# Performance work log

Hardware: AMD Instinct MI355X
Metric: run time of the kernel (lower is better)

Reference implementation:

```python
import jax, jax.numpy as jnp
import numpy as np

E, H, F, LE, LD, K, CD, DIN = 256, 8, 1024, 4, 3, 8, 4, 4
B, S = 16, 512
SIG2 = 1.0 ** 2 + 1e-8   # dr_sigma**2 + 1e-8
EPS = 1e-5               # LayerNorm / BatchNorm eps


def _ln(x, w, b):
    m = x.mean(-1, keepdims=True)
    v = ((x - m) ** 2).mean(-1, keepdims=True)
    return (x - m) / jnp.sqrt(v + EPS) * w + b


def _gelu(x):
    return jax.nn.gelu(x, approximate=False)  # torch nn.GELU default = exact erf


def _mha(xq, xkv, qkv_w, qkv_b, out_w, out_b, bias=None):
    # torch nn.MultiheadAttention (batch_first), additive float attn bias broadcast over heads
    wq, wk, wv = jnp.split(qkv_w, 3, axis=0)
    bq, bk, bv = jnp.split(qkv_b, 3)
    q = xq @ wq.T + bq
    k = xkv @ wk.T + bk
    v = xkv @ wv.T + bv
    Bn, Tq, Tk = q.shape[0], q.shape[1], k.shape[1]
    hd = E // H
    qh = q.reshape(Bn, Tq, H, hd)
    kh = k.reshape(Bn, Tk, H, hd)
    vh = v.reshape(Bn, Tk, H, hd)
    s = jnp.einsum('bqhd,bkhd->bhqk', qh, kh) / jnp.sqrt(jnp.asarray(hd, q.dtype))
    if bias is not None:
        s = s + bias[:, None]  # same bias for every head
    p = jax.nn.softmax(s, axis=-1)
    o = jnp.einsum('bhqk,bkhd->bqhd', p, vh).reshape(Bn, Tq, E)
    return o @ out_w.T + out_b


def _forward(x, mask, parent_idx, in_w, in_b, bn_w, bn_b, dr_gamma,
             e_qkv_w, e_qkv_b, e_out_w, e_out_b, e_l1_w, e_l1_b, e_l2_w, e_l2_b,
             e_n1_w, e_n1_b, e_n2_w, e_n2_b,
             parent_w, parent_b, query_embed, c1_w, c1_b, c2_w, c2_b,
             d_sqkv_w, d_sqkv_b, d_sout_w, d_sout_b,
             d_cqkv_w, d_cqkv_b, d_cout_w, d_cout_b,
             d_l1_w, d_l1_b, d_l2_w, d_l2_b,
             d_n1_w, d_n1_b, d_n2_w, d_n2_b, d_n3_w, d_n3_b,
             child_w, child_b, o1_w, o1_b, o2_w, o2_b):
    x = jnp.nan_to_num(x)
    # input_dim==4 convention: (log_pt, dEta, dPhi, log_E)
    coords = jnp.stack([x[..., 1], x[..., 2]], axis=-1)          # [B,S,2]
    # input_proj: Linear -> BatchNorm1d (eval: mean 0, var 1) -> GELU (dropout=identity in eval)
    h = x @ in_w.T + in_b
    h = (h / jnp.sqrt(1.0 + EPS)) * bn_w + bn_b
    h = _gelu(h)
    # dR Gaussian attention bias: [B,S,S]; mask is all-valid so no -inf fill
    d = coords[:, :, None, :] - coords[:, None, :, :]
    dr2 = d[..., 0] ** 2 + d[..., 1] ** 2
    bias = -(dr_gamma[0] * dr2) / (2.0 * SIG2)
    # dR-biased pre-norm encoder
    for i in range(LE):
        hn = _ln(h, e_n1_w[i], e_n1_b[i])
        h = h + _mha(hn, hn, e_qkv_w[i], e_qkv_b[i], e_out_w[i], e_out_b[i], bias)
        hn = _ln(h, e_n2_w[i], e_n2_b[i])
        h = h + _gelu(hn @ e_l1_w[i].T + e_l1_b[i]) @ e_l2_w[i].T + e_l2_b[i]
    memory = jnp.nan_to_num(h)
    parent_logit = (memory @ parent_w.T + parent_b)[..., 0]       # [B,S]
    # conditional decoder queries
    p = memory[jnp.arange(memory.shape[0]), parent_idx]           # [B,E]
    m = mask.astype(memory.dtype)
    g = (memory * m[..., None]).sum(1) / jnp.maximum(m.sum(1, keepdims=True), 1.0)
    cond = _gelu(jnp.concatenate([p, g], -1) @ c1_w.T + c1_b) @ c2_w.T + c2_b
    t = query_embed[None] + cond[:, None]                         # [B,K,E]
    # pre-norm transformer decoder (self-attn, cross-attn, ff)
    for i in range(LD):
        tn = _ln(t, d_n1_w[i], d_n1_b[i])
        t = t + _mha(tn, tn, d_sqkv_w[i], d_sqkv_b[i], d_sout_w[i], d_sout_b[i])
        tn = _ln(t, d_n2_w[i], d_n2_b[i])
        t = t + _mha(tn, memory, d_cqkv_w[i], d_cqkv_b[i], d_cout_w[i], d_cout_b[i])
        tn = _ln(t, d_n3_w[i], d_n3_b[i])
        t = t + _gelu(tn @ d_l1_w[i].T + d_l1_b[i]) @ d_l2_w[i].T + d_l2_b[i]
    child_feat = t @ child_w.T + child_b                          # [B,K,CD]
    obj_logit = (_gelu(t @ o1_w.T + o1_b) @ o2_w.T + o2_b)[..., 0]  # [B,K]
    return parent_logit, child_feat, obj_logit


def setup_inputs() -> dict:
    key = jax.random.key(0)
    ks = iter(jax.random.split(key, 64))
    def w(shape, scale=0.05):
        return jax.random.normal(next(ks), shape, jnp.float32) * scale
    return {
        'x': jax.random.normal(next(ks), (B, S, DIN), jnp.float32),
        'mask': jnp.ones((B, S), dtype=bool),
        'parent_idx': jax.random.randint(next(ks), (B,), 0, S),
        'in_w': w((E, DIN)), 'in_b': jnp.zeros((E,)),
        'bn_w': jnp.ones((E,)), 'bn_b': jnp.zeros((E,)),
        'dr_gamma': jnp.ones((1,)),
        'e_qkv_w': w((LE, 3 * E, E)), 'e_qkv_b': jnp.zeros((LE, 3 * E)),
        'e_out_w': w((LE, E, E)), 'e_out_b': jnp.zeros((LE, E)),
        'e_l1_w': w((LE, F, E)), 'e_l1_b': jnp.zeros((LE, F)),
        'e_l2_w': w((LE, E, F)), 'e_l2_b': jnp.zeros((LE, E)),
        'e_n1_w': jnp.ones((LE, E)), 'e_n1_b': jnp.zeros((LE, E)),
        'e_n2_w': jnp.ones((LE, E)), 'e_n2_b': jnp.zeros((LE, E)),
        'parent_w': w((1, E)), 'parent_b': jnp.zeros((1,)),
        'query_embed': w((K, E), 0.02),
        'c1_w': w((E, 2 * E)), 'c1_b': jnp.zeros((E,)),
        'c2_w': w((E, E)), 'c2_b': jnp.zeros((E,)),
        'd_sqkv_w': w((LD, 3 * E, E)), 'd_sqkv_b': jnp.zeros((LD, 3 * E)),
        'd_sout_w': w((LD, E, E)), 'd_sout_b': jnp.zeros((LD, E)),
        'd_cqkv_w': w((LD, 3 * E, E)), 'd_cqkv_b': jnp.zeros((LD, 3 * E)),
        'd_cout_w': w((LD, E, E)), 'd_cout_b': jnp.zeros((LD, E)),
        'd_l1_w': w((LD, F, E)), 'd_l1_b': jnp.zeros((LD, F)),
        'd_l2_w': w((LD, E, F)), 'd_l2_b': jnp.zeros((LD, E)),
        'd_n1_w': jnp.ones((LD, E)), 'd_n1_b': jnp.zeros((LD, E)),
        'd_n2_w': jnp.ones((LD, E)), 'd_n2_b': jnp.zeros((LD, E)),
        'd_n3_w': jnp.ones((LD, E)), 'd_n3_b': jnp.zeros((LD, E)),
        'child_w': w((CD, E)), 'child_b': jnp.zeros((CD,)),
        'o1_w': w((E, E)), 'o1_b': jnp.zeros((E,)),
        'o2_w': w((1, E)), 'o2_b': jnp.zeros((1,)),
    }


def reference(x, mask, parent_idx, in_w, in_b, bn_w, bn_b, dr_gamma,
              e_qkv_w, e_qkv_b, e_out_w, e_out_b, e_l1_w, e_l1_b, e_l2_w, e_l2_b,
              e_n1_w, e_n1_b, e_n2_w, e_n2_b,
              parent_w, parent_b, query_embed, c1_w, c1_b, c2_w, c2_b,
              d_sqkv_w, d_sqkv_b, d_sout_w, d_sout_b,
              d_cqkv_w, d_cqkv_b, d_cout_w, d_cout_b,
              d_l1_w, d_l1_b, d_l2_w, d_l2_b,
              d_n1_w, d_n1_b, d_n2_w, d_n2_b, d_n3_w, d_n3_b,
              child_w, child_b, o1_w, o1_b, o2_w, o2_b):
    return _forward(x, mask, parent_idx, in_w, in_b, bn_w, bn_b, dr_gamma,
                    e_qkv_w, e_qkv_b, e_out_w, e_out_b, e_l1_w, e_l1_b, e_l2_w, e_l2_b,
                    e_n1_w, e_n1_b, e_n2_w, e_n2_b,
                    parent_w, parent_b, query_embed, c1_w, c1_b, c2_w, c2_b,
                    d_sqkv_w, d_sqkv_b, d_sout_w, d_sout_b,
                    d_cqkv_w, d_cqkv_b, d_cout_w, d_cout_b,
                    d_l1_w, d_l1_b, d_l2_w, d_l2_b,
                    d_n1_w, d_n1_b, d_n2_w, d_n2_b, d_n3_w, d_n3_b,
                    child_w, child_b, o1_w, o1_b, o2_w, o2_b)
```

## Files before the change

### kernel.cpp

```cpp
#include <hip/hip_runtime.h>
#include <math.h>

#define E 256
#define H 8
#define HD 32
#define FF 1024
#define LE 4
#define LDN 3
#define KQ 8
#define CDIM 4
#define DIN 4
#define BATCH 16
#define SEQ 512

typedef __attribute__((ext_vector_type(8))) short s8b;
typedef __attribute__((ext_vector_type(4))) float f32x4;

__device__ __forceinline__ float gelu_f(float x) {
  return 0.5f * x * (1.f + erff(x * 0.70710678118654752f));
}

__device__ __forceinline__ unsigned short f2b(float f) {
  union { float f; unsigned u; } a;
  a.f = f;
  unsigned r = (a.u + 0x7fffu + ((a.u >> 16) & 1u)) >> 16;
  return (unsigned short)r;
}

template <int GELU, int RESID, int OMODE>
__global__ __launch_bounds__(256) void mfma_gemm_kernel(
    const unsigned short* __restrict__ A, const unsigned short* __restrict__ Wt,
    const float* __restrict__ bias, const float* __restrict__ resid,
    float* __restrict__ outf, unsigned short* __restrict__ outb,
    unsigned short* __restrict__ vtb,
    int M, int N, int K) {
  __shared__ unsigned short As[128 * 32];
  __shared__ unsigned short Bs[128 * 32];
  int tid = threadIdx.x;
  int lane = tid & 63, w = tid >> 6;
  int row0 = blockIdx.y * 128, col0 = blockIdx.x * 128;
  int wr = (w >> 1) * 64, wc = (w & 1) * 64;
  f32x4 acc[4][4] = {};
  int sr = tid >> 2;
  int sc = tid & 3;
  const unsigned short* Ap = A + (size_t)(row0 + sr) * K + sc * 8;
  const unsigned short* Bp = Wt + (size_t)(col0 + sr) * K + sc * 8;
  int xw = (sc ^ ((sr >> 1) & 3)) * 8;
  int w0 = sr * 32 + xw;
  int w1 = (sr + 64) * 32 + xw;

  for (int k0 = 0; k0 < K; k0 += 32) {
    s8b a0 = *(const s8b*)(Ap + k0);
    s8b a1 = *(const s8b*)(Ap + (size_t)64 * K + k0);
    s8b b0 = *(const s8b*)(Bp + k0);
    s8b b1 = *(const s8b*)(Bp + (size_t)64 * K + k0);
    __syncthreads();
    *(s8b*)(As + w0) = a0;
    *(s8b*)(As + w1) = a1;
    *(s8b*)(Bs + w0) = b0;
    *(s8b*)(Bs + w1) = b1;
    __syncthreads();
    int krow = lane & 15, kq = lane >> 4;
    s8b afr[4], bfr[4];
    #pragma unroll
    for (int mi = 0; mi < 4; ++mi) {
      int r = wr + mi * 16 + krow;
      afr[mi] = *(const s8b*)(As + r * 32 + ((kq ^ ((r >> 1) & 3)) * 8));
    }
    #pragma unroll
    for (int ni = 0; ni < 4; ++ni) {
      int r = wc + ni * 16 + krow;
      bfr[ni] = *(const s8b*)(Bs + r * 32 + ((kq ^ ((r >> 1) & 3)) * 8));
    }
    #pragma unroll
    for (int mi = 0; mi < 4; ++mi)
      #pragma unroll
      for (int ni = 0; ni < 4; ++ni)
        acc[mi][ni] = __builtin_amdgcn_mfma_f32_16x16x32_bf16(afr[mi], bfr[ni], acc[mi][ni], 0, 0, 0);
  }

  int cl = lane & 15, rb = (lane >> 4) * 4;
  #pragma unroll
  for (int ni = 0; ni < 4; ++ni) {
    int col = col0 + wc + ni * 16 + cl;
    float bv = bias[col];
    #pragma unroll
    for (int mi = 0; mi < 4; ++mi) {
      #pragma unroll
      for (int j = 0; j < 4; ++j) {
        int row = row0 + wr + mi * 16 + rb + j;
        float v = acc[mi][ni][j] + bv;
        if (RESID) v += resid[(size_t)row * N + col];
        if (GELU) v = gelu_f(v);
        if (OMODE == 0) {
          outf[(size_t)row * N + col] = v;
        } else if (OMODE == 1) {
          outb[(size_t)row * N + col] = f2b(v);
        } else {
          int b = row >> 9, s = row & 511;
          int sect = col >> 8, hh = (col >> 5) & 7, d = col & 31;
          if (sect < 2)
            outb[((((size_t)sect * BATCH + b) * H + hh) * SEQ + s) * HD + d] = f2b(v);
          else
            vtb[(((size_t)b * H + hh) * HD + d) * SEQ + s] = f2b(v);
        }
      }
    }
  }
}

__global__ __launch_bounds__(256) void mfma_attn_kernel(
    const unsigned short* __restrict__ qkb, const unsigned short* __restrict__ vt,
    const float2* __restrict__ carr, const float* __restrict__ gamma_p,
    unsigned short* __restrict__ out) {
  __shared__ __align__(16) unsigned short P[4][16 * 64];
  int tid = threadIdx.x, lane = tid & 63, w = tid >> 6;
  int qt = blockIdx.x, h = blockIdx.y, b = blockIdx.z;
  int q0 = qt * 64 + w * 16;
  const unsigned short* qh = qkb + (((size_t)b * H + h) * SEQ) * HD;
  const unsigned short* kh = qkb + ((((size_t)BATCH + b) * H + h) * SEQ) * HD;
  const unsigned short* vh = vt + (((size_t)b * H + h) * HD) * SEQ;
  int r16 = lane & 15, q4 = lane >> 4;
  s8b qa = *(const s8b*)(qh + (size_t)(q0 + r16) * HD + q4 * 8);
  float eq[4], pq[4];
  #pragma unroll
  for (int j = 0; j < 4; ++j) {
    float2 c = carr[b * SEQ + q0 + q4 * 4 + j];
    eq[j] = c.x; pq[j] = c.y;
  }
  float gam = gamma_p[0] * 0.49999999500000004f;
  const float scale = 0.17677669529663687f;
  float m[4], lsum[4];
  #pragma unroll
  for (int j = 0; j < 4; ++j) { m[j] = -1e30f; lsum[j] = 0.f; }
  f32x4 o0 = {}, o1 = {};
  const f32x4 zf = {0.f, 0.f, 0.f, 0.f};
  unsigned short* pw = &P[w][0];

  for (int t = 0; t < SEQ / 64; ++t) {
    int k0 = t * 64;
    f32x4 sf[4];
    #pragma unroll
    for (int f = 0; f < 4; ++f) {
      s8b bk = *(const s8b*)(kh + (size_t)(k0 + f * 16 + r16) * HD + q4 * 8);
      sf[f] = __builtin_amdgcn_mfma_f32_16x16x32_bf16(qa, bk, zf, 0, 0, 0);
    }
    float ek[4], pk[4];
    #pragma unroll
    for (int f = 0; f < 4; ++f) {
      float2 c = carr[b * SEQ + k0 + f * 16 + r16];
      ek[f] = c.x; pk[f] = c.y;
    }
    float sc_[4][4];
    float tmax[4] = {-1e30f, -1e30f, -1e30f, -1e30f};
    #pragma unroll
    for (int f = 0; f < 4; ++f)
      #pragma unroll
      for (int j = 0; j < 4; ++j) {
        float de = eq[j] - ek[f], dp = pq[j] - pk[f];
        float v = sf[f][j] * scale - gam * (de * de + dp * dp);
        sc_[f][j] = v;
        tmax[j] = fmaxf(tmax[j], v);
      }
    #pragma unroll
    for (int j = 0; j < 4; ++j) {
      #pragma unroll
      for (int off = 1; off < 16; off <<= 1)
        tmax[j] = fmaxf(tmax[j], __shfl_xor(tmax[j], off));
      float mn = fmaxf(m[j], tmax[j]);
      float al = __expf(m[j] - mn);
      m[j] = mn;
      lsum[j] *= al;
      o0[j] *= al;
      o1[j] *= al;
    }
    __syncthreads();
    #pragma unroll
    for (int f = 0; f < 4; ++f)
      #pragma unroll
      for (int j = 0; j < 4; ++j) {
        float p = __expf(sc_[f][j] - m[j]);
        lsum[j] += p;
        int prow = q4 * 4 + j;
        int c = f * 16 + r16;
        int chunk = (c >> 3) ^ (prow & 7);
        pw[prow * 64 + chunk * 8 + (c & 7)] = f2b(p);
      }
    __syncthreads();
    #pragma unroll
    for (int ks = 0; ks < 2; ++ks) {
      int chunk = (ks * 4 + q4) ^ (r16 & 7);
      s8b pa = *(const s8b*)(pw + r16 * 64 + chunk * 8);
      s8b v0 = *(const s8b*)(vh + (size_t)r16 * SEQ + k0 + ks * 32 + q4 * 8);
      s8b v1 = *(const s8b*)(vh + (size_t)(16 + r16) * SEQ + k0 + ks * 32 + q4 * 8);
      o0 = __builtin_amdgcn_mfma_f32_16x16x32_bf16(pa, v0, o0, 0, 0, 0);
      o1 = __builtin_amdgcn_mfma_f32_16x16x32_bf16(pa, v1, o1, 0, 0, 0);
    }
  }
  #pragma unroll
  for (int j = 0; j < 4; ++j) {
    #pragma unroll
    for (int off = 1; off < 16; off <<= 1)
      lsum[j] += __shfl_xor(lsum[j], off);
    float inv = 1.f / lsum[j];
    size_t rbase = ((size_t)(b * SEQ + q0 + q4 * 4 + j)) * E + h * HD;
    out[rbase + r16] = f2b(o0[j] * inv);
    out[rbase + 16 + r16] = f2b(o1[j] * inv);
  }
}

__global__ void coords_kernel(const float* __restrict__ x, float2* __restrict__ carr) {
  int i = blockIdx.x * 256 + threadIdx.x;
  if (i >= BATCH * SEQ) return;
  carr[i] = make_float2(x[(size_t)i * DIN + 1], x[(size_t)i * DIN + 2]);
}

__global__ void f2b_kernel(const float* __restrict__ in, unsigned short* __restrict__ out, int n4) {
  int i = blockIdx.x * 256 + threadIdx.x;
  if (i >= n4) return;
  float4 v = ((const float4*)in)[i];
  ushort4 o;
  o.x = f2b(v.x); o.y = f2b(v.y); o.z = f2b(v.z); o.w = f2b(v.w);
  ((ushort4*)out)[i] = o;
}


template <int N, int GELU>
__global__ __launch_bounds__(256) void dec_ln_gemv_kernel(
    const float* __restrict__ t, const float* __restrict__ nw, const float* __restrict__ nb,
    const float* __restrict__ W, const float* __restrict__ bias, float* __restrict__ outg) {
  __shared__ float X[8][256];
  __shared__ float Pp[4][64][9];
  int b = blockIdx.x, by = blockIdx.y, tid = threadIdx.x;
  const float* tg = t + (size_t)b * 2048;
  int w = tid >> 6, l = tid & 63;
  #pragma unroll
  for (int rr = 0; rr < 2; ++rr) {
    int r = w * 2 + rr;
    float v0 = tg[r * 256 + l], v1 = tg[r * 256 + 64 + l];
    float v2 = tg[r * 256 + 128 + l], v3 = tg[r * 256 + 192 + l];
    float s = v0 + v1 + v2 + v3;
    for (int o = 32; o > 0; o >>= 1) s += __shfl_xor(s, o);
    float mean = s * (1.f / 256);
    float d0 = v0 - mean, d1 = v1 - mean, d2 = v2 - mean, d3 = v3 - mean;
    float var = d0 * d0 + d1 * d1 + d2 * d2 + d3 * d3;
    for (int o = 32; o > 0; o >>= 1) var += __shfl_xor(var, o);
    float inv = rsqrtf(var * (1.f / 256) + 1e-5f);
    X[r][l] = d0 * inv * nw[l] + nb[l];
    X[r][l + 64] = d1 * inv * nw[l + 64] + nb[l + 64];
    X[r][l + 128] = d2 * inv * nw[l + 128] + nb[l + 128];
    X[r][l + 192] = d3 * inv * nw[l + 192] + nb[l + 192];
  }
  __syncthreads();
  int j = tid & 63, kq = tid >> 6;
  int col = by * 64 + j;
  const float4* wp = (const float4*)(W + (size_t)col * 256 + kq * 64);
  float acc[8] = {};
  #pragma unroll
  for (int kk = 0; kk < 16; ++kk) {
    float4 wv = wp[kk];
    int base = kq * 64 + kk * 4;
    #pragma unroll
    for (int r = 0; r < 8; ++r) {
      float4 xv = *(const float4*)&X[r][base];
      acc[r] += xv.x * wv.x + xv.y * wv.y + xv.z * wv.z + xv.w * wv.w;
    }
  }
  #pragma unroll
  for (int r = 0; r < 8; ++r) Pp[kq][j][r] = acc[r];
  __syncthreads();
  for (int i = tid; i < 512; i += 256) {
    int r = i & 7, j2 = i >> 3;
    float v = Pp[0][j2][r] + Pp[1][j2][r] + Pp[2][j2][r] + Pp[3][j2][r] + bias[by * 64 + j2];
    if (GELU) v = gelu_f(v);
    outg[((size_t)b * 8 + r) * N + by * 64 + j2] = v;
  }
}

__global__ __launch_bounds__(256) void dec_gemv_resid_kernel(
    const float* __restrict__ Xg, const float* __restrict__ W, const float* __restrict__ bias,
    float* __restrict__ t) {
  __shared__ float X[8][256];
  __shared__ float Pp[4][64][9];
  int b = blockIdx.x, by = blockIdx.y, tid = threadIdx.x;
  const float* xg = Xg + (size_t)b * 2048;
  for (int i = tid; i < 2048; i += 256) ((float*)X)[i] = xg[i];
  __syncthreads();
  int j = tid & 63, kq = tid >> 6;
  int col = by * 64 + j;
  const float4* wp = (const float4*)(W + (size_t)col * 256 + kq * 64);
  float acc[8] = {};
  #pragma unroll
  for (int kk = 0; kk < 16; ++kk) {
    float4 wv = wp[kk];
    int base = kq * 64 + kk * 4;
    #pragma unroll
    for (int r = 0; r < 8; ++r) {
      float4 xv = *(const float4*)&X[r][base];
      acc[r] += xv.x * wv.x + xv.y * wv.y + xv.z * wv.z + xv.w * wv.w;
    }
  }
  #pragma unroll
  for (int r = 0; r < 8; ++r) Pp[kq][j][r] = acc[r];
  __syncthreads();
  for (int i = tid; i < 512; i += 256) {
    int r = i & 7, j2 = i >> 3;
    float v = Pp[0][j2][r] + Pp[1][j2][r] + Pp[2][j2][r] + Pp[3][j2][r] + bias[by * 64 + j2];
    t[((size_t)b * 8 + r) * 256 + by * 64 + j2] += v;
  }
}

__global__ __launch_bounds__(256) void dec_ffn2_kernel(
    const float* __restrict__ MIDg, const float* __restrict__ W, const float* __restrict__ bias,
    float* __restrict__ t) {
  __shared__ float X[8][1024];
  __shared__ float Pp[4][64][9];
  int b = blockIdx.x, by = blockIdx.y, tid = threadIdx.x;
  const float* xg = MIDg + (size_t)b * 8192;
  for (int i = tid; i < 8192; i += 256) ((float*)X)[i] = xg[i];
  __syncthreads();
  int j = tid & 63, kq = tid >> 6;
  int col = by * 64 + j;
  const float4* wp = (const float4*)(W + (size_t)col * 1024 + kq * 256);
  float acc[8] = {};
  #pragma unroll 8
  for (int kk = 0; kk < 64; ++kk) {
    float4 wv = wp[kk];
    int base = kq * 256 + kk * 4;
    #pragma unroll
    for (int r = 0; r < 8; ++r) {
      float4 xv = *(const float4*)&X[r][base];
      acc[r] += xv.x * wv.x + xv.y * wv.y + xv.z * wv.z + xv.w * wv.w;
    }
  }
  #pragma unroll
  for (int r = 0; r < 8; ++r) Pp[kq][j][r] = acc[r];
  __syncthreads();
  for (int i = tid; i < 512; i += 256) {
    int r = i & 7, j2 = i >> 3;
    float v = Pp[0][j2][r] + Pp[1][j2][r] + Pp[2][j2][r] + Pp[3][j2][r] + bias[by * 64 + j2];
    t[((size_t)b * 8 + r) * 256 + by * 64 + j2] += v;
  }
}

__global__ __launch_bounds__(256) void dec_selfattn_kernel(
    const float* __restrict__ qkvg, float* __restrict__ ao) {
  __shared__ float QK[8][768];
  __shared__ float S[512];
  int b = blockIdx.x, tid = threadIdx.x;
  const float* qg = qkvg + (size_t)b * 8 * 768;
  for (int i = tid; i < 6144; i += 256) ((float*)QK)[i] = qg[i];
  __syncthreads();
  for (int t2 = tid; t2 < 512; t2 += 256) {
    int h = t2 >> 6, q = (t2 >> 3) & 7, k = t2 & 7;
    const float* qp = &QK[q][h * 32];
    const float* kp = &QK[k][256 + h * 32];
    float d = 0.f;
    #pragma unroll
    for (int jj = 0; jj < 32; ++jj) d += qp[jj] * kp[jj];
    S[t2] = d * 0.17677669529663687f;
  }
  __syncthreads();
  if (tid < 64) {
    float* row = &S[tid * 8];
    float m = row[0];
    #pragma unroll
    for (int k = 1; k < 8; ++k) m = fmaxf(m, row[k]);
    float sum = 0.f;
    #pragma unroll
    for (int k = 0; k < 8; ++k) { float e = __expf(row[k] - m); row[k] = e; sum += e; }
    float inv = 1.f / sum;
    #pragma unroll
    for (int k = 0; k < 8; ++k) row[k] *= inv;
  }
  __syncthreads();
  for (int i = tid; i < 2048; i += 256) {
    int q = i >> 8, c = i & 255, h = c >> 5;
    const float* pr = &S[h * 64 + q * 8];
    float acc = 0.f;
    #pragma unroll
    for (int k = 0; k < 8; ++k) acc += pr[k] * QK[k][512 + c];
    ao[(size_t)b * 2048 + i] = acc;
  }
}

__global__ void cross_attn_kernel(const float* __restrict__ Q,
                                  const float* __restrict__ KV,
                                  float* __restrict__ out) {
  __shared__ float sv[512];
  __shared__ float red[256];
  __shared__ float qv[32];
  __shared__ float pvred[8][32];
  int tid = threadIdx.x;
  int bid = blockIdx.x;
  int q = bid % KQ;
  int h = (bid / KQ) % H;
  int b = bid / (KQ * H);
  if (tid < 32) qv[tid] = Q[((size_t)(b * KQ + q)) * E + h * HD + tid];
  __syncthreads();
  const float scale = 0.17677669529663687f;
  for (int k = tid; k < SEQ; k += 256) {
    const float* kp = KV + ((size_t)(b * SEQ + k)) * 512 + h * HD;
    float d = 0.f;
    #pragma unroll
    for (int j = 0; j < HD; ++j) d += qv[j] * kp[j];
    sv[k] = d * scale;
  }
  __syncthreads();
  float m = -1e30f;
  for (int k = tid; k < SEQ; k += 256) m = fmaxf(m, sv[k]);
  red[tid] = m; __syncthreads();
  for (int s = 128; s > 0; s >>= 1) {
    if (tid < s) red[tid] = fmaxf(red[tid], red[tid + s]);
    __syncthreads();
  }
  m = red[0]; __syncthreads();
  float lsum = 0.f;
  for (int k = tid; k < SEQ; k += 256) { float e = __expf(sv[k] - m); sv[k] = e; lsum += e; }
  red[tid] = lsum; __syncthreads();
  for (int s = 128; s > 0; s >>= 1) {
    if (tid < s) red[tid] += red[tid + s];
    __syncthreads();
  }
  float denom = red[0];
  int d = tid & 31, g = tid >> 5;
  float acc = 0.f;
  for (int k = g; k < SEQ; k += 8)
    acc += sv[k] * KV[((size_t)(b * SEQ + k)) * 512 + 256 + h * HD + d];
  pvred[g][d] = acc;
  __syncthreads();
  if (tid < 32) {
    float r = 0.f;
    #pragma unroll
    for (int gg = 0; gg < 8; ++gg) r += pvred[gg][tid];
    out[((size_t)(b * KQ + q)) * E + h * HD + tid] = r / denom;
  }
}

__global__ void ln_bf16_kernel(const float* __restrict__ in, const float* __restrict__ w,
                               const float* __restrict__ b, unsigned short* __restrict__ out) {
  int r = blockIdx.x;
  int l = threadIdx.x;
  const float* p = in + (size_t)r * E;
  float v0 = p[l], v1 = p[l + 64], v2 = p[l + 128], v3 = p[l + 192];
  float s = v0 + v1 + v2 + v3;
  for (int off = 32; off > 0; off >>= 1) s += __shfl_xor(s, off);
  float mean = s * (1.f / E);
  float d0 = v0 - mean, d1 = v1 - mean, d2 = v2 - mean, d3 = v3 - mean;
  float var = d0 * d0 + d1 * d1 + d2 * d2 + d3 * d3;
  for (int off = 32; off > 0; off >>= 1) var += __shfl_xor(var, off);
  float inv = rsqrtf(var * (1.f / E) + 1e-5f);
  unsigned short* o = out + (size_t)r * E;
  o[l]       = f2b(d0 * inv * w[l]       + b[l]);
  o[l + 64]  = f2b(d1 * inv * w[l + 64]  + b[l + 64]);
  o[l + 128] = f2b(d2 * inv * w[l + 128] + b[l + 128]);
  o[l + 192] = f2b(d3 * inv * w[l + 192] + b[l + 192]);
}

__global__ void input_proj_kernel(const float* __restrict__ x, const float* __restrict__ in_w,
                                  const float* __restrict__ in_b, const float* __restrict__ bn_w,
                                  const float* __restrict__ bn_b, float* __restrict__ h) {
  int idx = blockIdx.x * 256 + threadIdx.x;
  int row = idx >> 8, e = idx & 255;
  const float* xr = x + (size_t)row * DIN;
  float v = in_b[e];
  #pragma unroll
  for (int i = 0; i < DIN; ++i) v += xr[i] * in_w[e * DIN + i];
  v = v * (1.0f / sqrtf(1.0f + 1e-5f)) * bn_w[e] + bn_b[e];
  h[idx] = gelu_f(v);
}

__global__ void pool_gather_kernel(const float* __restrict__ mem, const int* __restrict__ pidx,
                                   float* __restrict__ pg) {
  int b = blockIdx.x, e = threadIdx.x;
  int pi = pidx[b];
  pg[(size_t)b * 512 + e] = mem[((size_t)b * SEQ + pi) * E + e];
  float s = 0.f;
  #pragma unroll 8
  for (int ss = 0; ss < SEQ; ++ss) s += mem[((size_t)b * SEQ + ss) * E + e];
  pg[(size_t)b * 512 + 256 + e] = s * (1.f / SEQ);
}

__global__ void cond_kernel(const float* __restrict__ pg, const float* __restrict__ c1w,
                            const float* __restrict__ c1b, const float* __restrict__ c2w,
                            const float* __restrict__ c2b, const float* __restrict__ qe,
                            float* __restrict__ t) {
  __shared__ float PG[512];
  __shared__ float C1[256];
  int b = blockIdx.x, c = threadIdx.x;
  PG[c] = pg[(size_t)b * 512 + c];
  PG[c + 256] = pg[(size_t)b * 512 + 256 + c];
  __syncthreads();
  const float4* wp = (const float4*)(c1w + (size_t)c * 512);
  float acc = c1b[c];
  #pragma unroll 8
  for (int kk = 0; kk < 128; ++kk) {
    float4 wv = wp[kk];
    int base = kk * 4;
    acc += PG[base] * wv.x + PG[base + 1] * wv.y + PG[base + 2] * wv.z + PG[base + 3] * wv.w;
  }
  C1[c] = gelu_f(acc);
  __syncthreads();
  const float4* wp2 = (const float4*)(c2w + (size_t)c * 256);
  float acc2 = c2b[c];
  #pragma unroll 8
  for (int kk = 0; kk < 64; ++kk) {
    float4 wv = wp2[kk];
    int base = kk * 4;
    acc2 += C1[base] * wv.x + C1[base + 1] * wv.y + C1[base + 2] * wv.z + C1[base + 3] * wv.w;
  }
  #pragma unroll
  for (int k = 0; k < KQ; ++k)
    t[((size_t)b * KQ + k) * E + c] = qe[k * E + c] + acc2;
}

__global__ void head_kernel(const float* __restrict__ t,
                            const float* __restrict__ childw, const float* __restrict__ childb,
                            const float* __restrict__ o1w, const float* __restrict__ o1b,
                            const float* __restrict__ o2w, const float* __restrict__ o2b,
                            float* __restrict__ out_child, float* __restrict__ out_obj) {
  __shared__ float tr[256];
  __shared__ float red[256];
  int r = blockIdx.x, c = threadIdx.x;
  tr[c] = t[(size_t)r * E + c];
  __syncthreads();
  const float4* wp = (const float4*)(o1w + (size_t)c * 256);
  float acc = o1b[c];
  #pragma unroll 8
  for (int kk = 0; kk < 64; ++kk) {
    float4 wv = wp[kk];
    int base = kk * 4;
    acc += tr[base] * wv.x + tr[base + 1] * wv.y + tr[base + 2] * wv.z + tr[base + 3] * wv.w;
  }
  red[c] = gelu_f(acc) * o2w[c];
  __syncthreads();
  for (int s = 128; s > 0; s >>= 1) {
    if (c < s) red[c] += red[c + s];
    __syncthreads();
  }
  if (c == 0) out_obj[r] = red[0] + o2b[0];
  __syncthreads();
  #pragma unroll
  for (int j = 0; j < CDIM; ++j) {
    red[c] = tr[c] * childw[j * E + c];
    __syncthreads();
    for (int s = 128; s > 0; s >>= 1) {
      if (c < s) red[c] += red[c + s];
      __syncthreads();
    }
    if (c == 0) out_child[r * CDIM + j] = red[0] + childb[j];
    __syncthreads();
  }
}

__global__ void rowdot_kernel(const float* __restrict__ A, const float* __restrict__ w,
                              const float* __restrict__ bias, float* __restrict__ out) {
  int r = blockIdx.x, l = threadIdx.x;
  const float* p = A + (size_t)r * E;
  float s = p[l] * w[l] + p[l + 64] * w[l + 64] + p[l + 128] * w[l + 128] + p[l + 192] * w[l + 192];
  for (int off = 32; off > 0; off >>= 1) s += __shfl_xor(s, off);
  if (l == 0) out[r] = s + bias[0];
}

extern "C" void kernel_launch(void* const* d_in, const int* in_sizes, int n_in,
                              void* d_out, int out_size, void* d_ws, size_t ws_size,
                              hipStream_t stream) {
  const float* x          = (const float*)d_in[0];
  const int*   parent_idx = (const int*)d_in[2];
  const float* in_w  = (const float*)d_in[3];
  const float* in_b  = (const float*)d_in[4];
  const float* bn_w  = (const float*)d_in[5];
  const float* bn_b  = (const float*)d_in[6];
  const float* dr_gamma = (const float*)d_in[7];
  const float* e_qkv_w = (const float*)d_in[8];
  const float* e_qkv_b = (const float*)d_in[9];
  const float* e_out_w = (const float*)d_in[10];
  const float* e_out_b = (const float*)d_in[11];
  const float* e_l1_w = (const float*)d_in[12];
  const float* e_l1_b = (const float*)d_in[13];
  const float* e_l2_w = (const float*)d_in[14];
  const float* e_l2_b = (const float*)d_in[15];
  const float* e_n1_w = (const float*)d_in[16];
  const float* e_n1_b = (const float*)d_in[17];
  const float* e_n2_w = (const float*)d_in[18];
  const float* e_n2_b = (const float*)d_in[19];
  const float* parent_w = (const float*)d_in[20];
  const float* parent_b = (const float*)d_in[21];
  const float* query_embed = (const float*)d_in[22];
  const float* c1_w = (const float*)d_in[23];
  const float* c1_b = (const float*)d_in[24];
  const float* c2_w = (const float*)d_in[25];
  const float* c2_b = (const float*)d_in[26];
  const float* d_sqkv_w = (const float*)d_in[27];
  const float* d_sqkv_b = (const float*)d_in[28];
  const float* d_sout_w = (const float*)d_in[29];
  const float* d_sout_b = (const float*)d_in[30];
  const float* d_cqkv_w = (const float*)d_in[31];
  const float* d_cqkv_b = (const float*)d_in[32];
  const float* d_cout_w = (const float*)d_in[33];
  const float* d_cout_b = (const float*)d_in[34];
  const float* d_l1_w = (const float*)d_in[35];
  const float* d_l1_b = (const float*)d_in[36];
  const float* d_l2_w = (const float*)d_in[37];
  const float* d_l2_b = (const float*)d_in[38];
  const float* d_n1_w = (const float*)d_in[39];
  const float* d_n1_b = (const float*)d_in[40];
  const float* d_n2_w = (const float*)d_in[41];
  const float* d_n2_b = (const float*)d_in[42];
  const float* d_n3_w = (const float*)d_in[43];
  const float* d_n3_b = (const float*)d_in[44];
  const float* child_w = (const float*)d_in[45];
  const float* child_b = (const float*)d_in[46];
  const float* o1_w = (const float*)d_in[47];
  const float* o1_b = (const float*)d_in[48];
  const float* o2_w = (const float*)d_in[49];
  const float* o2_b = (const float*)d_in[50];

  float* out = (float*)d_out;
  const int ROWS = BATCH * SEQ;
  const int TROWS = BATCH * KQ;

  float* ws = (float*)d_ws;
  float* h         = ws;
  float* kvbuf     = h + (size_t)ROWS * E;
  float* attnout_d = kvbuf + (size_t)ROWS * 2 * E;
  float* pg        = attnout_d + (size_t)TROWS * E;
  float* tbuf      = pg + BATCH * 2 * E;
  float* q_t       = tbuf + (size_t)TROWS * E;
  float* qkv_t     = q_t + (size_t)TROWS * E;
  float* dmid      = qkv_t + (size_t)TROWS * 3 * E;
  unsigned short* hn_bf   = (unsigned short*)(dmid + (size_t)TROWS * FF);
  unsigned short* attn_bf = hn_bf + (size_t)ROWS * E;
  unsigned short* mid_bf  = attn_bf + (size_t)ROWS * E;
  unsigned short* eqkv_bf = mid_bf + (size_t)ROWS * FF;
  unsigned short* eout_bf = eqkv_bf + (size_t)LE * 3 * E * E;
  unsigned short* el1_bf  = eout_bf + (size_t)LE * E * E;
  unsigned short* el2_bf  = el1_bf + (size_t)LE * FF * E;
  unsigned short* dckv_bf = el2_bf + (size_t)LE * E * FF;
  float2* carr = (float2*)(dckv_bf + (size_t)LDN * 3 * E * E);
  unsigned short* qkb = mid_bf;
  unsigned short* vtb = mid_bf + (size_t)2 * ROWS * E;

  auto cvt = [&](const float* src, unsigned short* dst, size_t n) {
    int n4 = (int)(n / 4);
    f2b_kernel<<<(n4 + 255) / 256, 256, 0, stream>>>(src, dst, n4);
  };

  cvt(e_qkv_w, eqkv_bf, (size_t)LE * 3 * E * E);
  cvt(e_out_w, eout_bf, (size_t)LE * E * E);
  cvt(e_l1_w, el1_bf, (size_t)LE * FF * E);
  cvt(e_l2_w, el2_bf, (size_t)LE * E * FF);
  cvt(d_cqkv_w, dckv_bf, (size_t)LDN * 3 * E * E);
  coords_kernel<<<(BATCH * SEQ + 255) / 256, 256, 0, stream>>>(x, carr);

  input_proj_kernel<<<ROWS, 256, 0, stream>>>(x, in_w, in_b, bn_w, bn_b, h);

  for (int i = 0; i < LE; ++i) {
    const float* qb = e_qkv_b + (size_t)i * 3 * E;
    const float* ob = e_out_b + (size_t)i * E;
    const float* l1b = e_l1_b + (size_t)i * FF;
    const float* l2b = e_l2_b + (size_t)i * E;
    ln_bf16_kernel<<<ROWS, 64, 0, stream>>>(h, e_n1_w + i * E, e_n1_b + i * E, hn_bf);
    mfma_gemm_kernel<0, 0, 2><<<dim3(6, 64), 256, 0, stream>>>(
        hn_bf, eqkv_bf + (size_t)i * 3 * E * E, qb, nullptr, nullptr, qkb, vtb, ROWS, 3 * E, E);
    mfma_attn_kernel<<<dim3(SEQ / 64, H, BATCH), 256, 0, stream>>>(qkb, vtb, carr, dr_gamma, attn_bf);
    mfma_gemm_kernel<0, 1, 0><<<dim3(2, 64), 256, 0, stream>>>(
        attn_bf, eout_bf + (size_t)i * E * E, ob, h, h, nullptr, nullptr, ROWS, E, E);
    ln_bf16_kernel<<<ROWS, 64, 0, stream>>>(h, e_n2_w + i * E, e_n2_b + i * E, hn_bf);
    mfma_gemm_kernel<1, 0, 1><<<dim3(8, 64), 256, 0, stream>>>(
        hn_bf, el1_bf + (size_t)i * FF * E, l1b, nullptr, nullptr, mid_bf, nullptr, ROWS, FF, E);
    mfma_gemm_kernel<0, 1, 0><<<dim3(2, 64), 256, 0, stream>>>(
        mid_bf, el2_bf + (size_t)i * E * FF, l2b, h, h, nullptr, nullptr, ROWS, E, FF);
  }

  rowdot_kernel<<<ROWS, 64, 0, stream>>>(h, parent_w, parent_b, out);

  pool_gather_kernel<<<BATCH, 256, 0, stream>>>(h, parent_idx, pg);
  cond_kernel<<<BATCH, 256, 0, stream>>>(pg, c1_w, c1_b, c2_w, c2_b, query_embed, tbuf);

  cvt(h, hn_bf, (size_t)ROWS * E);

  for (int i = 0; i < LDN; ++i) {
    const float* cqb = d_cqkv_b + (size_t)i * 3 * E;
    mfma_gemm_kernel<0, 0, 0><<<dim3(4, 64), 256, 0, stream>>>(
        hn_bf, dckv_bf + (size_t)i * 3 * E * E + (size_t)E * E, cqb + E, nullptr,
        kvbuf, nullptr, nullptr, ROWS, 2 * E, E);
    dec_ln_gemv_kernel<768, 0><<<dim3(BATCH, 12), 256, 0, stream>>>(
        tbuf, d_n1_w + i * E, d_n1_b + i * E,
        d_sqkv_w + (size_t)i * 3 * E * E, d_sqkv_b + (size_t)i * 3 * E, qkv_t);
    dec_selfattn_kernel<<<BATCH, 256, 0, stream>>>(qkv_t, attnout_d);
    dec_gemv_resid_kernel<<<dim3(BATCH, 4), 256, 0, stream>>>(
        attnout_d, d_sout_w + (size_t)i * E * E, d_sout_b + (size_t)i * E, tbuf);
    dec_ln_gemv_kernel<256, 0><<<dim3(BATCH, 4), 256, 0, stream>>>(
        tbuf, d_n2_w + i * E, d_n2_b + i * E,
        d_cqkv_w + (size_t)i * 3 * E * E, cqb, q_t);
    cross_attn_kernel<<<BATCH * H * KQ, 256, 0, stream>>>(q_t, kvbuf, attnout_d);
    dec_gemv_resid_kernel<<<dim3(BATCH, 4), 256, 0, stream>>>(
        attnout_d, d_cout_w + (size_t)i * E * E, d_cout_b + (size_t)i * E, tbuf);
    dec_ln_gemv_kernel<1024, 1><<<dim3(BATCH, 16), 256, 0, stream>>>(
        tbuf, d_n3_w + i * E, d_n3_b + i * E,
        d_l1_w + (size_t)i * FF * E, d_l1_b + (size_t)i * FF, dmid);
    dec_ffn2_kernel<<<dim3(BATCH, 4), 256, 0, stream>>>(
        dmid, d_l2_w + (size_t)i * E * FF, d_l2_b + (size_t)i * E, tbuf);
  }

  head_kernel<<<TROWS, 256, 0, stream>>>(tbuf, child_w, child_b, o1_w, o1_b, o2_w, o2_b,
                                         out + ROWS, out + ROWS + TROWS * CDIM);
}
```

Before: 866.1 us.

## Use direct global-to-LDS loads, batch decoder KV GEMMs, parallelize pooling

The GEMM tile loads now use global_load_lds to write straight into shared memory, with the swizzle moved to the global address side, so staging no longer passes through registers. The three decoder cross-attention K/V projections are merged into one wide GEMM over remapped bf16 weights, and cross-attention indexes them by stride and offset. The mean-pool/gather kernel is split across feature chunks to use more blocks. The direct LDS loads depend on correct lane-to-address mapping, and the merged GEMM adds a larger fp32 buffer.

```diff
diff --git a/kernel.cpp b/kernel.cpp
--- a/kernel.cpp
+++ b/kernel.cpp
@@ -27,6 +27,11 @@
   return (unsigned short)r;
 }
 
+__device__ __forceinline__ void gload16(const unsigned short* g, unsigned short* l) {
+  __builtin_amdgcn_global_load_lds((const __attribute__((address_space(1))) void*)g,
+                                   (__attribute__((address_space(3))) void*)l, 16, 0, 0);
+}
+
 template <int GELU, int RESID, int OMODE>
 __global__ __launch_bounds__(256) void mfma_gemm_kernel(
     const unsigned short* __restrict__ A, const unsigned short* __restrict__ Wt,
@@ -34,31 +39,34 @@
     float* __restrict__ outf, unsigned short* __restrict__ outb,
     unsigned short* __restrict__ vtb,
     int M, int N, int K) {
-  __shared__ unsigned short As[128 * 32];
-  __shared__ unsigned short Bs[128 * 32];
+  __shared__ __align__(16) unsigned short As[128 * 32];
+  __shared__ __align__(16) unsigned short Bs[128 * 32];
   int tid = threadIdx.x;
   int lane = tid & 63, w = tid >> 6;
   int row0 = blockIdx.y * 128, col0 = blockIdx.x * 128;
   int wr = (w >> 1) * 64, wc = (w & 1) * 64;
   f32x4 acc[4][4] = {};
-  int sr = tid >> 2;
-  int sc = tid & 3;
-  const unsigned short* Ap = A + (size_t)(row0 + sr) * K + sc * 8;
-  const unsigned short* Bp = Wt + (size_t)(col0 + sr) * K + sc * 8;
-  int xw = (sc ^ ((sr >> 1) & 3)) * 8;
-  int w0 = sr * 32 + xw;
-  int w1 = (sr + 64) * 32 + xw;
+
+  int sr0 = w * 32 + (lane >> 2);
+  int sr1 = sr0 + 16;
+  int sc = lane & 3;
+  int gc0 = (sc ^ ((sr0 >> 1) & 3)) * 8;
+  int gc1 = (sc ^ ((sr1 >> 1) & 3)) * 8;
+  const unsigned short* Ap0 = A + (size_t)(row0 + sr0) * K + gc0;
+  const unsigned short* Ap1 = A + (size_t)(row0 + sr1) * K + gc1;
+  const unsigned short* Bp0 = Wt + (size_t)(col0 + sr0) * K + gc0;
+  const unsigned short* Bp1 = Wt + (size_t)(col0 + sr1) * K + gc1;
+  unsigned short* lA0 = As + (w * 32) * 32;
+  unsigned short* lA1 = As + (w * 32 + 16) * 32;
+  unsigned short* lB0 = Bs + (w * 32) * 32;
+  unsigned short* lB1 = Bs + (w * 32 + 16) * 32;
 
   for (int k0 = 0; k0 < K; k0 += 32) {
-    s8b a0 = *(const s8b*)(Ap + k0);
-    s8b a1 = *(const s8b*)(Ap + (size_t)64 * K + k0);
-    s8b b0 = *(const s8b*)(Bp + k0);
-    s8b b1 = *(const s8b*)(Bp + (size_t)64 * K + k0);
-    __syncthreads();
-    *(s8b*)(As + w0) = a0;
-    *(s8b*)(As + w1) = a1;
-    *(s8b*)(Bs + w0) = b0;
-    *(s8b*)(Bs + w1) = b1;
+    __syncthreads();
+    gload16(Ap0 + k0, lA0);
+    gload16(Ap1 + k0, lA1);
+    gload16(Bp0 + k0, lB0);
+    gload16(Bp1 + k0, lB1);
     __syncthreads();
     int krow = lane & 15, kq = lane >> 4;
     s8b afr[4], bfr[4];
@@ -224,6 +232,20 @@
   ((ushort4*)out)[i] = o;
 }
 
+__global__ void kvw_remap_kernel(const float* __restrict__ w, const float* __restrict__ b,
+                                 unsigned short* __restrict__ wout, float* __restrict__ bout) {
+  int i = blockIdx.x * 256 + threadIdx.x;
+  if (i < 1536) bout[i] = b[(i >> 9) * 768 + 256 + (i & 511)];
+  if (i >= 98304) return;
+  int row = i >> 6, cc = i & 63;
+  int l = row >> 9, rr = row & 511;
+  const float* src = w + ((size_t)l * 768 + 256 + rr) * 256 + cc * 4;
+  float4 v = *(const float4*)src;
+  ushort4 o;
+  o.x = f2b(v.x); o.y = f2b(v.y); o.z = f2b(v.z); o.w = f2b(v.w);
+  *(ushort4*)(wout + (size_t)row * 256 + cc * 4) = o;
+}
+
 
 template <int N, int GELU>
 __global__ __launch_bounds__(256) void dec_ln_gemv_kernel(
@@ -385,7 +407,7 @@
 }
 
 __global__ void cross_attn_kernel(const float* __restrict__ Q,
-                                  const float* __restrict__ KV,
+                                  const float* __restrict__ KV, int kvstride, int koff, int voff,
                                   float* __restrict__ out) {
   __shared__ float sv[512];
   __shared__ float red[256];
@@ -400,7 +422,7 @@
   __syncthreads();
   const float scale = 0.17677669529663687f;
   for (int k = tid; k < SEQ; k += 256) {
-    const float* kp = KV + ((size_t)(b * SEQ + k)) * 512 + h * HD;
+    const float* kp = KV + ((size_t)(b * SEQ + k)) * kvstride + koff + h * HD;
     float d = 0.f;
     #pragma unroll
     for (int j = 0; j < HD; ++j) d += qv[j] * kp[j];
@@ -426,7 +448,7 @@
   int d = tid & 31, g = tid >> 5;
   float acc = 0.f;
   for (int k = g; k < SEQ; k += 8)
-    acc += sv[k] * KV[((size_t)(b * SEQ + k)) * 512 + 256 + h * HD + d];
+    acc += sv[k] * KV[((size_t)(b * SEQ + k)) * kvstride + voff + h * HD + d];
   pvred[g][d] = acc;
   __syncthreads();
   if (tid < 32) {
@@ -470,15 +492,23 @@
   h[idx] = gelu_f(v);
 }
 
-__global__ void pool_gather_kernel(const float* __restrict__ mem, const int* __restrict__ pidx,
-                                   float* __restrict__ pg) {
-  int b = blockIdx.x, e = threadIdx.x;
-  int pi = pidx[b];
-  pg[(size_t)b * 512 + e] = mem[((size_t)b * SEQ + pi) * E + e];
+__global__ __launch_bounds__(256) void pool_gather_kernel(
+    const float* __restrict__ mem, const int* __restrict__ pidx, float* __restrict__ pg) {
+  __shared__ float red[8][32];
+  int b = blockIdx.x, cy = blockIdx.y, tid = threadIdx.x;
+  int c = cy * 32 + (tid & 31), g = tid >> 5;
   float s = 0.f;
-  #pragma unroll 8
-  for (int ss = 0; ss < SEQ; ++ss) s += mem[((size_t)b * SEQ + ss) * E + e];
-  pg[(size_t)b * 512 + 256 + e] = s * (1.f / SEQ);
+  for (int r = g; r < SEQ; r += 8)
+    s += mem[((size_t)b * SEQ + r) * E + c];
+  red[g][tid & 31] = s;
+  __syncthreads();
+  if (tid < 32) {
+    float t = 0.f;
+    #pragma unroll
+    for (int g2 = 0; g2 < 8; ++g2) t += red[g2][tid];
+    pg[(size_t)b * 512 + 256 + cy * 32 + tid] = t * (1.f / SEQ);
+    pg[(size_t)b * 512 + cy * 32 + tid] = mem[((size_t)b * SEQ + pidx[b]) * E + cy * 32 + tid];
+  }
 }
 
 __global__ void cond_kernel(const float* __restrict__ pg, const float* __restrict__ c1w,
@@ -622,22 +652,23 @@
 
   float* ws = (float*)d_ws;
   float* h         = ws;
-  float* kvbuf     = h + (size_t)ROWS * E;
-  float* attnout_d = kvbuf + (size_t)ROWS * 2 * E;
+  float* kv3       = h + (size_t)ROWS * E;
+  float* attnout_d = kv3 + (size_t)ROWS * 3 * E * 2;
   float* pg        = attnout_d + (size_t)TROWS * E;
   float* tbuf      = pg + BATCH * 2 * E;
   float* q_t       = tbuf + (size_t)TROWS * E;
   float* qkv_t     = q_t + (size_t)TROWS * E;
   float* dmid      = qkv_t + (size_t)TROWS * 3 * E;
-  unsigned short* hn_bf   = (unsigned short*)(dmid + (size_t)TROWS * FF);
+  float* kvb3      = dmid + (size_t)TROWS * FF;
+  unsigned short* hn_bf   = (unsigned short*)(kvb3 + 1536);
   unsigned short* attn_bf = hn_bf + (size_t)ROWS * E;
   unsigned short* mid_bf  = attn_bf + (size_t)ROWS * E;
   unsigned short* eqkv_bf = mid_bf + (size_t)ROWS * FF;
   unsigned short* eout_bf = eqkv_bf + (size_t)LE * 3 * E * E;
   unsigned short* el1_bf  = eout_bf + (size_t)LE * E * E;
   unsigned short* el2_bf  = el1_bf + (size_t)LE * FF * E;
-  unsigned short* dckv_bf = el2_bf + (size_t)LE * E * FF;
-  float2* carr = (float2*)(dckv_bf + (size_t)LDN * 3 * E * E);
+  unsigned short* kvw_bf  = el2_bf + (size_t)LE * E * FF;
+  float2* carr = (float2*)(kvw_bf + (size_t)1536 * 256);
   unsigned short* qkb = mid_bf;
   unsigned short* vtb = mid_bf + (size_t)2 * ROWS * E;
 
@@ -650,7 +681,7 @@
   cvt(e_out_w, eout_bf, (size_t)LE * E * E);
   cvt(e_l1_w, el1_bf, (size_t)LE * FF * E);
   cvt(e_l2_w, el2_bf, (size_t)LE * E * FF);
-  cvt(d_cqkv_w, dckv_bf, (size_t)LDN * 3 * E * E);
+  kvw_remap_kernel<<<384, 256, 0, stream>>>(d_cqkv_w, d_cqkv_b, kvw_bf, kvb3);
   coords_kernel<<<(BATCH * SEQ + 255) / 256, 256, 0, stream>>>(x, carr);
 
   input_proj_kernel<<<ROWS, 256, 0, stream>>>(x, in_w, in_b, bn_w, bn_b, h);
@@ -675,16 +706,14 @@
 
   rowdot_kernel<<<ROWS, 64, 0, stream>>>(h, parent_w, parent_b, out);
 
-  pool_gather_kernel<<<BATCH, 256, 0, stream>>>(h, parent_idx, pg);
+  pool_gather_kernel<<<dim3(BATCH, 8), 256, 0, stream>>>(h, parent_idx, pg);
   cond_kernel<<<BATCH, 256, 0, stream>>>(pg, c1_w, c1_b, c2_w, c2_b, query_embed, tbuf);
 
   cvt(h, hn_bf, (size_t)ROWS * E);
+  mfma_gemm_kernel<0, 0, 0><<<dim3(12, 64), 256, 0, stream>>>(
+      hn_bf, kvw_bf, kvb3, nullptr, kv3, nullptr, nullptr, ROWS, 3 * E * 2, E);
 
   for (int i = 0; i < LDN; ++i) {
-    const float* cqb = d_cqkv_b + (size_t)i * 3 * E;
-    mfma_gemm_kernel<0, 0, 0><<<dim3(4, 64), 256, 0, stream>>>(
-        hn_bf, dckv_bf + (size_t)i * 3 * E * E + (size_t)E * E, cqb + E, nullptr,
-        kvbuf, nullptr, nullptr, ROWS, 2 * E, E);
     dec_ln_gemv_kernel<768, 0><<<dim3(BATCH, 12), 256, 0, stream>>>(
         tbuf, d_n1_w + i * E, d_n1_b + i * E,
         d_sqkv_w + (size_t)i * 3 * E * E, d_sqkv_b + (size_t)i * 3 * E, qkv_t);
@@ -693,8 +722,9 @@
         attnout_d, d_sout_w + (size_t)i * E * E, d_sout_b + (size_t)i * E, tbuf);
     dec_ln_gemv_kernel<256, 0><<<dim3(BATCH, 4), 256, 0, stream>>>(
         tbuf, d_n2_w + i * E, d_n2_b + i * E,
-        d_cqkv_w + (size_t)i * 3 * E * E, cqb, q_t);
-    cross_attn_kernel<<<BATCH * H * KQ, 256, 0, stream>>>(q_t, kvbuf, attnout_d);
+        d_cqkv_w + (size_t)i * 3 * E * E, d_cqkv_b + (size_t)i * 3 * E, q_t);
+    cross_attn_kernel<<<BATCH * H * KQ, 256, 0, stream>>>(
+        q_t, kv3, 1536, i * 512, i * 512 + 256, attnout_d);
     dec_gemv_resid_kernel<<<dim3(BATCH, 4), 256, 0, stream>>>(
         attnout_d, d_cout_w + (size_t)i * E * E, d_cout_b + (size_t)i * E, tbuf);
     dec_ln_gemv_kernel<1024, 1><<<dim3(BATCH, 16), 256, 0, stream>>>(
```

Result: no change. 857.6 us (-1.0%).
